# Kernel tuning notes

Hardware: AMD Instinct MI355X
Metric: run time of the kernel (lower is better)

Reference implementation:

```python
import jax, jax.numpy as jnp
import numpy as np

N = 8192
IN = 128   # in_channels
CH = 64    # conv_ch


def setup_inputs() -> dict:
    key = jax.random.key(0)
    ks = jax.random.split(key, 8)
    p = lambda k, shape: jax.random.normal(k, shape, jnp.float32) * 0.02
    return {
        "x": jax.random.normal(ks[0], (N, IN), jnp.float32),
        "edge_index": jax.random.randint(ks[1], (N, N), 0, 2, jnp.int32),
        "W1": p(ks[2], (IN, CH)),      "b1": jnp.zeros((CH,), jnp.float32),
        "W2": p(ks[3], (CH, 2 * CH)),  "b2": jnp.zeros((2 * CH,), jnp.float32),
        "We": p(ks[4], (2 * CH, CH)),  "be": jnp.zeros((CH,), jnp.float32),
        "Wd1": p(ks[5], (2 * CH, CH)), "bd1": jnp.zeros((CH,), jnp.float32),
        "Wd2": p(ks[6], (CH, IN)),     "bd2": jnp.zeros((IN,), jnp.float32),
    }


def _norm_adj(edge_index):
    # PyG GCNConv: A_hat = A + I (self loops appended), sym norm D^-1/2 A_hat D^-1/2
    A = (edge_index != 0).astype(jnp.float32)
    A = A + jnp.eye(A.shape[0], dtype=jnp.float32)
    deg = A.sum(axis=1)
    dinv = jnp.where(deg > 0.0, jax.lax.rsqrt(deg), 0.0)
    return dinv[:, None] * A * dinv[None, :]  # [N, N]


def _gcn(nadj, x, W, b):
    return nadj @ (x @ W) + b


def _lrelu(v):
    return jax.nn.leaky_relu(v, 0.01)  # torch default negative_slope


def reference(x, edge_index, W1, b1, W2, b2, We, be, Wd1, bd1, Wd2, bd2):
    nadj = _norm_adj(edge_index)
    h = _lrelu(_gcn(nadj, x, W1, b1))          # [N, CH]
    z = _lrelu(_gcn(nadj, h, W2, b2))          # [N, 2*CH]
    re = _lrelu(_gcn(nadj, z, We, be))         # [N, CH]
    recon_edge = jax.nn.sigmoid(re @ re.T)     # [N, N]
    xd = _lrelu(_gcn(nadj, z, Wd1, bd1))       # [N, CH]
    x_out = _lrelu(_gcn(nadj, xd, Wd2, bd2))   # [N, IN]
    return (recon_edge, x_out, z)
```

## Files before the change

kernel.cpp:

```cpp
#include <hip/hip_runtime.h>
#include <hip/hip_bf16.h>
#include <stdint.h>

typedef unsigned short u16;
typedef __attribute__((ext_vector_type(8))) short frag8;
typedef __attribute__((ext_vector_type(4))) float f4;

#define N8K 8192
#define SK 8

__device__ __forceinline__ u16 f2bf(float f) {
  union { float f; unsigned u; } v; v.f = f;
  return (u16)((v.u + 0x7FFFu + ((v.u >> 16) & 1u)) >> 16);
}
__device__ __forceinline__ float lrelu(float v) { return v > 0.f ? v : 0.01f * v; }

__device__ __forceinline__ void gld16(const void* g, void* l) {
  __builtin_amdgcn_global_load_lds(
      (__attribute__((address_space(1))) unsigned*)(g),
      (__attribute__((address_space(3))) unsigned*)(l), 16, 0, 0);
}

__global__ __launch_bounds__(256) void k_deg(const int* __restrict__ e,
                                             u16* __restrict__ abf,
                                             float* __restrict__ dinv) {
  int row = blockIdx.x;
  int t = threadIdx.x;
  const int4* er = (const int4*)(e + (size_t)row * N8K);
  ushort4* ar = (ushort4*)(abf + (size_t)row * N8K);
  int cnt = 0;
#pragma unroll
  for (int it = 0; it < 8; ++it) {
    int j4 = it * 256 + t;
    int4 v = er[j4];
    int col = j4 << 2;
    int c0 = (v.x != 0), c1 = (v.y != 0), c2 = (v.z != 0), c3 = (v.w != 0);
    cnt += c0 + c1 + c2 + c3;
    ushort4 a;
    a.x = c0 ? 0x3F80u : 0u;
    a.y = c1 ? 0x3F80u : 0u;
    a.z = c2 ? 0x3F80u : 0u;
    a.w = c3 ? 0x3F80u : 0u;
    if (row >= col && row < col + 4) {
      u16* ap = (u16*)&a;
      int d = row - col;
      ap[d] = ap[d] ? 0x4000u : 0x3F80u;
      cnt += 1;
    }
    ar[j4] = a;
  }
#pragma unroll
  for (int o = 32; o > 0; o >>= 1) cnt += __shfl_down(cnt, o);
  __shared__ int part[4];
  if ((t & 63) == 0) part[t >> 6] = cnt;
  __syncthreads();
  if (t == 0) dinv[row] = 1.0f / sqrtf((float)(part[0] + part[1] + part[2] + part[3]));
}

__global__ __launch_bounds__(256) void k_cvt(const float* __restrict__ x, u16* __restrict__ xb, int n) {
  int i = blockIdx.x * 256 + threadIdx.x;
  if (i < n) xb[i] = f2bf(x[i]);
}

__global__ __launch_bounds__(256) void k_sgemm(const u16* __restrict__ X, int kc, int lkc,
                                               const float* __restrict__ Wa, int wacols,
                                               const float* __restrict__ Wb,
                                               const float* __restrict__ dinv,
                                               u16* __restrict__ Pt) {
  __shared__ __attribute__((aligned(16))) u16 Xs[128 * 128];
  __shared__ __attribute__((aligned(16))) u16 Wt[128 * 128];
  int t = threadIdx.x;
  int mt = blockIdx.x;
  for (int idx = t; idx < (kc << 7); idx += 256) {
    int n = idx >> lkc, k = idx & (kc - 1);
    float v = 0.f;
    if (n < wacols) v = Wa[k * wacols + n];
    else if (Wb)    v = Wb[k * 64 + (n - 64)];
    Wt[(n << lkc) + k] = f2bf(v);
  }
  const u16* gX = X + (size_t)mt * 128 * kc;
  if (kc == 128) {
#pragma unroll
    for (int p = 0; p < 8; ++p) {
      int rr = p * 16 + (t >> 4), sg = t & 15;
      gld16(gX + rr * 128 + sg * 8, Xs + rr * 128 + sg * 8);
    }
  } else {
#pragma unroll
    for (int p = 0; p < 4; ++p) {
      int rr = p * 32 + (t >> 3), sg = t & 7;
      gld16(gX + rr * 64 + sg * 8, Xs + rr * 64 + sg * 8);
    }
  }
  __syncthreads();
  int wave = t >> 6, lane = t & 63;
  int wm = (wave >> 1) * 64, wn = (wave & 1) * 64;
  int fm = lane & 15, fk = (lane >> 4) * 8;
  f4 acc[4][4];
#pragma unroll
  for (int m = 0; m < 4; ++m)
#pragma unroll
    for (int n = 0; n < 4; ++n) acc[m][n] = (f4){0.f, 0.f, 0.f, 0.f};
  for (int ki = 0; ki < kc; ki += 32) {
    frag8 a[4], b[4];
#pragma unroll
    for (int m = 0; m < 4; ++m) a[m] = *(const frag8*)&Xs[(wm + 16 * m + fm) * kc + ki + fk];
#pragma unroll
    for (int n = 0; n < 4; ++n) b[n] = *(const frag8*)&Wt[((wn + 16 * n + fm) << lkc) + ki + fk];
#pragma unroll
    for (int m = 0; m < 4; ++m)
#pragma unroll
      for (int n = 0; n < 4; ++n)
        acc[m][n] = __builtin_amdgcn_mfma_f32_16x16x32_bf16(a[m], b[n], acc[m][n], 0, 0, 0);
  }
  int rbase = (lane >> 4) * 4;
#pragma unroll
  for (int m = 0; m < 4; ++m) {
    int i0 = mt * 128 + wm + 16 * m + rbase;
    float d0 = dinv[i0], d1 = dinv[i0 + 1], d2 = dinv[i0 + 2], d3 = dinv[i0 + 3];
#pragma unroll
    for (int n = 0; n < 4; ++n) {
      int c = wn + 16 * n + fm;
      ushort4 o;
      o.x = f2bf(d0 * acc[m][n][0]);
      o.y = f2bf(d1 * acc[m][n][1]);
      o.z = f2bf(d2 * acc[m][n][2]);
      o.w = f2bf(d3 * acc[m][n][3]);
      *(ushort4*)&Pt[(size_t)c * N8K + i0] = o;
    }
  }
}

__global__ __launch_bounds__(256) void k_bgemm(const u16* __restrict__ A,
                                               const u16* __restrict__ Pt,
                                               float* __restrict__ Ctmp) {
  __shared__ __attribute__((aligned(16))) u16 As[128 * 64];
  __shared__ __attribute__((aligned(16))) u16 Bs[128 * 64];
  int t = threadIdx.x;
  int mt = blockIdx.x, ks = blockIdx.y;
  const int KS = N8K / SK;
  int wave = t >> 6, lane = t & 63;
  int wm = (wave >> 1) * 64, wn = (wave & 1) * 64;
  int fm = lane & 15, fk = (lane >> 4) * 8;
  f4 acc[4][4];
#pragma unroll
  for (int m = 0; m < 4; ++m)
#pragma unroll
    for (int n = 0; n < 4; ++n) acc[m][n] = (f4){0.f, 0.f, 0.f, 0.f};

  int arow = t >> 3, aseg = t & 7;
  const u16* gA0 = A + (size_t)(mt * 128 + arow) * N8K + aseg * 8;
  const u16* gB0 = Pt + (size_t)arow * N8K + aseg * 8;
  u16* lA = As + arow * 64 + aseg * 8;
  u16* lB = Bs + arow * 64 + aseg * 8;

  for (int kk = ks * KS; kk < ks * KS + KS; kk += 64) {
    __syncthreads();
#pragma unroll
    for (int p = 0; p < 4; ++p) {
      gld16(gA0 + (size_t)p * 32 * N8K + kk, lA + p * 32 * 64);
      gld16(gB0 + (size_t)p * 32 * N8K + kk, lB + p * 32 * 64);
    }
    __syncthreads();
#pragma unroll
    for (int ki = 0; ki < 64; ki += 32) {
      frag8 a[4], b[4];
#pragma unroll
      for (int m = 0; m < 4; ++m) a[m] = *(const frag8*)&As[(wm + 16 * m + fm) * 64 + ki + fk];
#pragma unroll
      for (int n = 0; n < 4; ++n) b[n] = *(const frag8*)&Bs[(wn + 16 * n + fm) * 64 + ki + fk];
#pragma unroll
      for (int m = 0; m < 4; ++m)
#pragma unroll
        for (int n = 0; n < 4; ++n)
          acc[m][n] = __builtin_amdgcn_mfma_f32_16x16x32_bf16(a[m], b[n], acc[m][n], 0, 0, 0);
    }
  }
  float* Co = Ctmp + (size_t)ks * N8K * 128;
  int rbase = (lane >> 4) * 4;
#pragma unroll
  for (int m = 0; m < 4; ++m) {
    int i0 = mt * 128 + wm + 16 * m + rbase;
#pragma unroll
    for (int n = 0; n < 4; ++n) {
      int c = wn + 16 * n + fm;
#pragma unroll
      for (int r = 0; r < 4; ++r) Co[(size_t)(i0 + r) * 128 + c] = acc[m][n][r];
    }
  }
}

__global__ __launch_bounds__(256) void k_epi(const float* __restrict__ Ctmp, const float* __restrict__ dinv,
                                             const float* __restrict__ bA, const float* __restrict__ bB,
                                             float* __restrict__ outF, u16* __restrict__ oB1,
                                             u16* __restrict__ oB2, int mode) {
  int idx = blockIdx.x * 256 + threadIdx.x;
  int i = idx >> 7, c = idx & 127;
  float s = 0.f;
#pragma unroll
  for (int k = 0; k < SK; ++k) s += Ctmp[(size_t)k * 1048576 + idx];
  if (mode == 1) {
    if (c < 64) oB1[i * 64 + c] = f2bf(lrelu(dinv[i] * s + bA[c]));
  } else if (mode == 2) {
    float v = lrelu(dinv[i] * s + bA[c]);
    outF[idx] = v;
    oB1[idx] = f2bf(v);
  } else if (mode == 3) {
    if (c < 64) oB1[i * 64 + c] = f2bf(lrelu(dinv[i] * s + bA[c]));
    else        oB2[i * 64 + (c - 64)] = f2bf(lrelu(dinv[i] * s + bB[c - 64]));
  } else {
    outF[idx] = lrelu(dinv[i] * s + bA[c]);
  }
}

__global__ __launch_bounds__(256) void k_recon(const u16* __restrict__ re, float* __restrict__ out) {
  __shared__ __attribute__((aligned(16))) u16 Ra[128 * 64];
  __shared__ __attribute__((aligned(16))) u16 Rb[128 * 64];
  int t = threadIdx.x;
  int bi = blockIdx.x, bj = blockIdx.y;
  int r0 = t >> 3, sg = t & 7;
#pragma unroll
  for (int p = 0; p < 4; ++p) {
    int rr = p * 32 + r0;
    gld16(re + (size_t)(bi * 128 + rr) * 64 + sg * 8, Ra + rr * 64 + sg * 8);
    gld16(re + (size_t)(bj * 128 + rr) * 64 + sg * 8, Rb + rr * 64 + sg * 8);
  }
  __syncthreads();
  int wave = t >> 6, lane = t & 63;
  int wm = (wave >> 1) * 64, wn = (wave & 1) * 64;
  int fm = lane & 15, fk = (lane >> 4) * 8;
  f4 acc[4][4];
#pragma unroll
  for (int m = 0; m < 4; ++m)
#pragma unroll
    for (int n = 0; n < 4; ++n) acc[m][n] = (f4){0.f, 0.f, 0.f, 0.f};
#pragma unroll
  for (int ki = 0; ki < 64; ki += 32) {
    frag8 a[4], b[4];
#pragma unroll
    for (int m = 0; m < 4; ++m) a[m] = *(const frag8*)&Ra[(wm + 16 * m + fm) * 64 + ki + fk];
#pragma unroll
    for (int n = 0; n < 4; ++n) b[n] = *(const frag8*)&Rb[(wn + 16 * n + fm) * 64 + ki + fk];
#pragma unroll
    for (int m = 0; m < 4; ++m)
#pragma unroll
      for (int n = 0; n < 4; ++n)
        acc[m][n] = __builtin_amdgcn_mfma_f32_16x16x32_bf16(a[m], b[n], acc[m][n], 0, 0, 0);
  }
  int rbase = (lane >> 4) * 4;
#pragma unroll
  for (int m = 0; m < 4; ++m) {
#pragma unroll
    for (int n = 0; n < 4; ++n) {
      int gj = bj * 128 + wn + 16 * n + fm;
#pragma unroll
      for (int r = 0; r < 4; ++r) {
        int gi = bi * 128 + wm + 16 * m + rbase + r;
        float v = acc[m][n][r];
        out[(size_t)gi * N8K + gj] = 1.0f / (1.0f + __expf(-v));
      }
    }
  }
}

extern "C" void kernel_launch(void* const* d_in, const int* in_sizes, int n_in,
                              void* d_out, int out_size, void* d_ws, size_t ws_size,
                              hipStream_t stream) {
  const float* x   = (const float*)d_in[0];
  const int*   e   = (const int*)d_in[1];
  const float* W1  = (const float*)d_in[2];
  const float* b1  = (const float*)d_in[3];
  const float* W2  = (const float*)d_in[4];
  const float* b2  = (const float*)d_in[5];
  const float* We  = (const float*)d_in[6];
  const float* be  = (const float*)d_in[7];
  const float* Wd1 = (const float*)d_in[8];
  const float* bd1 = (const float*)d_in[9];
  const float* Wd2 = (const float*)d_in[10];
  const float* bd2 = (const float*)d_in[11];

  float* out       = (float*)d_out;
  float* out_recon = out;
  float* out_x     = out + 67108864;
  float* out_z     = out + 67108864 + 1048576;

  u16*   abf  = (u16*)d_out;
  float* Ctmp = out + 33554432;

  char* ws = (char*)d_ws;
  float* dinv = (float*)(ws);
  u16* Pt   = (u16*)(ws + 32768);
  u16* xbf  = (u16*)(ws + 32768 + 2097152);
  u16* hbf  = (u16*)(ws + 32768 + 2097152 + 2097152);
  u16* zbf  = (u16*)(ws + 32768 + 2097152 + 2097152 + 1048576);
  u16* rebf = (u16*)(ws + 32768 + 2097152 + 2097152 + 1048576 + 2097152);
  u16* xdbf = (u16*)(ws + 32768 + 2097152 + 2097152 + 1048576 + 2097152 + 1048576);

  k_deg<<<8192, 256, 0, stream>>>(e, abf, dinv);
  k_cvt<<<4096, 256, 0, stream>>>(x, xbf, 1048576);

  k_sgemm<<<64, 256, 0, stream>>>(xbf, 128, 7, W1, 64, nullptr, dinv, Pt);
  k_bgemm<<<dim3(64, SK), 256, 0, stream>>>(abf, Pt, Ctmp);
  k_epi<<<4096, 256, 0, stream>>>(Ctmp, dinv, b1, nullptr, nullptr, hbf, nullptr, 1);

  k_sgemm<<<64, 256, 0, stream>>>(hbf, 64, 6, W2, 128, nullptr, dinv, Pt);
  k_bgemm<<<dim3(64, SK), 256, 0, stream>>>(abf, Pt, Ctmp);
  k_epi<<<4096, 256, 0, stream>>>(Ctmp, dinv, b2, nullptr, out_z, zbf, nullptr, 2);

  k_sgemm<<<64, 256, 0, stream>>>(zbf, 128, 7, We, 64, Wd1, dinv, Pt);
  k_bgemm<<<dim3(64, SK), 256, 0, stream>>>(abf, Pt, Ctmp);
  k_epi<<<4096, 256, 0, stream>>>(Ctmp, dinv, be, bd1, nullptr, rebf, xdbf, 3);

  k_sgemm<<<64, 256, 0, stream>>>(xdbf, 64, 6, Wd2, 128, nullptr, dinv, Pt);
  k_bgemm<<<dim3(64, SK), 256, 0, stream>>>(abf, Pt, Ctmp);
  k_epi<<<4096, 256, 0, stream>>>(Ctmp, dinv, bd2, nullptr, out_x, nullptr, nullptr, 4);

  k_recon<<<dim3(64, 64), 256, 0, stream>>>(rebf, out_recon);
}
```

Before: 746.5 us.

## Pad bgemm LDS, register-prefetch next tile, stage recon output through LDS

The split-K bgemm kernel now pads its LDS rows to 72 elements to avoid bank conflicts. It replaces direct global-to-LDS loads with register prefetching of the next K tile, which overlaps global loads with MFMA compute. The recon kernel stages sigmoid results through an LDS buffer in 32-row chunks so each row is written to global memory as coalesced float4 stores instead of scattered scalar stores. The costs are extra LDS, extra VGPRs for the prefetch registers, and additional barriers in the recon epilogue.

```diff
diff --git a/kernel.cpp b/kernel.cpp
--- a/kernel.cpp
+++ b/kernel.cpp
@@ -8,6 +8,7 @@
 
 #define N8K 8192
 #define SK 8
+#define LDA 72
 
 __device__ __forceinline__ u16 f2bf(float f) {
   union { float f; unsigned u; } v; v.f = f;
@@ -134,8 +135,8 @@
 __global__ __launch_bounds__(256) void k_bgemm(const u16* __restrict__ A,
                                                const u16* __restrict__ Pt,
                                                float* __restrict__ Ctmp) {
-  __shared__ __attribute__((aligned(16))) u16 As[128 * 64];
-  __shared__ __attribute__((aligned(16))) u16 Bs[128 * 64];
+  __shared__ __attribute__((aligned(16))) u16 As[128 * LDA];
+  __shared__ __attribute__((aligned(16))) u16 Bs[128 * LDA];
   int t = threadIdx.x;
   int mt = blockIdx.x, ks = blockIdx.y;
   const int KS = N8K / SK;
@@ -151,24 +152,38 @@
   int arow = t >> 3, aseg = t & 7;
   const u16* gA0 = A + (size_t)(mt * 128 + arow) * N8K + aseg * 8;
   const u16* gB0 = Pt + (size_t)arow * N8K + aseg * 8;
-  u16* lA = As + arow * 64 + aseg * 8;
-  u16* lB = Bs + arow * 64 + aseg * 8;
-
-  for (int kk = ks * KS; kk < ks * KS + KS; kk += 64) {
+  u16* lA = As + arow * LDA + aseg * 8;
+  u16* lB = Bs + arow * LDA + aseg * 8;
+
+  int4 ra[4], rb[4];
+  int k0 = ks * KS, k1 = ks * KS + KS;
+#pragma unroll
+  for (int p = 0; p < 4; ++p) {
+    ra[p] = *(const int4*)(gA0 + (size_t)p * 32 * N8K + k0);
+    rb[p] = *(const int4*)(gB0 + (size_t)p * 32 * N8K + k0);
+  }
+  for (int kk = k0; kk < k1; kk += 64) {
     __syncthreads();
 #pragma unroll
     for (int p = 0; p < 4; ++p) {
-      gld16(gA0 + (size_t)p * 32 * N8K + kk, lA + p * 32 * 64);
-      gld16(gB0 + (size_t)p * 32 * N8K + kk, lB + p * 32 * 64);
+      *(int4*)(lA + p * 32 * LDA) = ra[p];
+      *(int4*)(lB + p * 32 * LDA) = rb[p];
     }
     __syncthreads();
+    if (kk + 64 < k1) {
+#pragma unroll
+      for (int p = 0; p < 4; ++p) {
+        ra[p] = *(const int4*)(gA0 + (size_t)p * 32 * N8K + kk + 64);
+        rb[p] = *(const int4*)(gB0 + (size_t)p * 32 * N8K + kk + 64);
+      }
+    }
 #pragma unroll
     for (int ki = 0; ki < 64; ki += 32) {
       frag8 a[4], b[4];
 #pragma unroll
-      for (int m = 0; m < 4; ++m) a[m] = *(const frag8*)&As[(wm + 16 * m + fm) * 64 + ki + fk];
-#pragma unroll
-      for (int n = 0; n < 4; ++n) b[n] = *(const frag8*)&Bs[(wn + 16 * n + fm) * 64 + ki + fk];
+      for (int m = 0; m < 4; ++m) a[m] = *(const frag8*)&As[(wm + 16 * m + fm) * LDA + ki + fk];
+#pragma unroll
+      for (int n = 0; n < 4; ++n) b[n] = *(const frag8*)&Bs[(wn + 16 * n + fm) * LDA + ki + fk];
 #pragma unroll
       for (int m = 0; m < 4; ++m)
 #pragma unroll
@@ -216,6 +231,7 @@
 __global__ __launch_bounds__(256) void k_recon(const u16* __restrict__ re, float* __restrict__ out) {
   __shared__ __attribute__((aligned(16))) u16 Ra[128 * 64];
   __shared__ __attribute__((aligned(16))) u16 Rb[128 * 64];
+  __shared__ __attribute__((aligned(16))) float Ls[32 * 132];
   int t = threadIdx.x;
   int bi = blockIdx.x, bj = blockIdx.y;
   int r0 = t >> 3, sg = t & 7;
@@ -249,16 +265,30 @@
   }
   int rbase = (lane >> 4) * 4;
 #pragma unroll
-  for (int m = 0; m < 4; ++m) {
-#pragma unroll
-    for (int n = 0; n < 4; ++n) {
-      int gj = bj * 128 + wn + 16 * n + fm;
-#pragma unroll
-      for (int r = 0; r < 4; ++r) {
-        int gi = bi * 128 + wm + 16 * m + rbase + r;
-        float v = acc[m][n][r];
-        out[(size_t)gi * N8K + gj] = 1.0f / (1.0f + __expf(-v));
+  for (int chunk = 0; chunk < 4; ++chunk) {
+    __syncthreads();
+    if (wm == (chunk >> 1) * 64) {
+      int mlo = (chunk & 1) * 2;
+#pragma unroll
+      for (int mm = 0; mm < 2; ++mm) {
+        int m = mlo + mm;
+        int lrow = (16 * m + rbase) & 31;
+#pragma unroll
+        for (int n = 0; n < 4; ++n) {
+          int col = wn + 16 * n + fm;
+#pragma unroll
+          for (int r = 0; r < 4; ++r)
+            Ls[(lrow + r) * 132 + col] = 1.0f / (1.0f + __expf(-acc[m][n][r]));
+        }
       }
+    }
+    __syncthreads();
+#pragma unroll
+    for (int it = 0; it < 4; ++it) {
+      int lr = it * 8 + (t >> 5);
+      int col = (t & 31) * 4;
+      float4 v = *(const float4*)&Ls[lr * 132 + col];
+      *(float4*)&out[(size_t)(bi * 128 + chunk * 32 + lr) * N8K + bj * 128 + col] = v;
     }
   }
 }
```

New measurement: 1.024 ms. +37.1%, slower.

## Store adjacency as bytes and expand to bf16 in registers for GCN GEMMs

Applied to the files above, without the earlier changes.

The normalized adjacency is now stored as one byte per entry (0, 1 or 2) instead of bf16, which halves the bytes the four aggregation GEMMs read. Bytes are widened to bf16 fragments in registers with byte-permute instructions. The aggregation and recon GEMMs drop LDS staging and load MFMA fragments straight from global memory. This gives up shared-memory tiling reuse and the barriers, and relies on caches for reuse of Pt and re across waves.

```diff
diff --git a/kernel.cpp b/kernel.cpp
--- a/kernel.cpp
+++ b/kernel.cpp
@@ -3,6 +3,8 @@
 #include <stdint.h>
 
 typedef unsigned short u16;
+typedef unsigned char u8;
+typedef unsigned int u32;
 typedef __attribute__((ext_vector_type(8))) short frag8;
 typedef __attribute__((ext_vector_type(4))) float f4;
 
@@ -21,33 +23,34 @@
       (__attribute__((address_space(3))) unsigned*)(l), 16, 0, 0);
 }
 
+__device__ __forceinline__ void expand4(u32 w, u32& o0, u32& o1) {
+  u32 hi = __builtin_amdgcn_perm(0u, 0x00403F00u, w);
+  u32 lo = __builtin_amdgcn_perm(0u, 0x00008000u, w);
+  o0 = __builtin_amdgcn_perm(hi, lo, 0x05010400u);
+  o1 = __builtin_amdgcn_perm(hi, lo, 0x07030602u);
+}
+
 __global__ __launch_bounds__(256) void k_deg(const int* __restrict__ e,
-                                             u16* __restrict__ abf,
+                                             u8* __restrict__ ab,
                                              float* __restrict__ dinv) {
   int row = blockIdx.x;
   int t = threadIdx.x;
   const int4* er = (const int4*)(e + (size_t)row * N8K);
-  ushort4* ar = (ushort4*)(abf + (size_t)row * N8K);
+  u32* ar = (u32*)(ab + (size_t)row * N8K);
   int cnt = 0;
 #pragma unroll
   for (int it = 0; it < 8; ++it) {
     int j4 = it * 256 + t;
     int4 v = er[j4];
     int col = j4 << 2;
-    int c0 = (v.x != 0), c1 = (v.y != 0), c2 = (v.z != 0), c3 = (v.w != 0);
-    cnt += c0 + c1 + c2 + c3;
-    ushort4 a;
-    a.x = c0 ? 0x3F80u : 0u;
-    a.y = c1 ? 0x3F80u : 0u;
-    a.z = c2 ? 0x3F80u : 0u;
-    a.w = c3 ? 0x3F80u : 0u;
+    u32 c0 = (v.x != 0), c1 = (v.y != 0), c2 = (v.z != 0), c3 = (v.w != 0);
+    cnt += (int)(c0 + c1 + c2 + c3);
+    u32 w = c0 | (c1 << 8) | (c2 << 16) | (c3 << 24);
     if (row >= col && row < col + 4) {
-      u16* ap = (u16*)&a;
-      int d = row - col;
-      ap[d] = ap[d] ? 0x4000u : 0x3F80u;
+      w += 1u << (8 * (row - col));
       cnt += 1;
     }
-    ar[j4] = a;
+    ar[j4] = w;
   }
 #pragma unroll
   for (int o = 32; o > 0; o >>= 1) cnt += __shfl_down(cnt, o);
@@ -131,11 +134,9 @@
   }
 }
 
-__global__ __launch_bounds__(256) void k_bgemm(const u16* __restrict__ A,
+__global__ __launch_bounds__(256) void k_bgemm(const u8* __restrict__ Ab,
                                                const u16* __restrict__ Pt,
                                                float* __restrict__ Ctmp) {
-  __shared__ __attribute__((aligned(16))) u16 As[128 * 64];
-  __shared__ __attribute__((aligned(16))) u16 Bs[128 * 64];
   int t = threadIdx.x;
   int mt = blockIdx.x, ks = blockIdx.y;
   const int KS = N8K / SK;
@@ -148,34 +149,30 @@
 #pragma unroll
     for (int n = 0; n < 4; ++n) acc[m][n] = (f4){0.f, 0.f, 0.f, 0.f};
 
-  int arow = t >> 3, aseg = t & 7;
-  const u16* gA0 = A + (size_t)(mt * 128 + arow) * N8K + aseg * 8;
-  const u16* gB0 = Pt + (size_t)arow * N8K + aseg * 8;
-  u16* lA = As + arow * 64 + aseg * 8;
-  u16* lB = Bs + arow * 64 + aseg * 8;
-
-  for (int kk = ks * KS; kk < ks * KS + KS; kk += 64) {
-    __syncthreads();
-#pragma unroll
-    for (int p = 0; p < 4; ++p) {
-      gld16(gA0 + (size_t)p * 32 * N8K + kk, lA + p * 32 * 64);
-      gld16(gB0 + (size_t)p * 32 * N8K + kk, lB + p * 32 * 64);
-    }
-    __syncthreads();
-#pragma unroll
-    for (int ki = 0; ki < 64; ki += 32) {
-      frag8 a[4], b[4];
-#pragma unroll
-      for (int m = 0; m < 4; ++m) a[m] = *(const frag8*)&As[(wm + 16 * m + fm) * 64 + ki + fk];
-#pragma unroll
-      for (int n = 0; n < 4; ++n) b[n] = *(const frag8*)&Bs[(wn + 16 * n + fm) * 64 + ki + fk];
-#pragma unroll
-      for (int m = 0; m < 4; ++m)
-#pragma unroll
-        for (int n = 0; n < 4; ++n)
-          acc[m][n] = __builtin_amdgcn_mfma_f32_16x16x32_bf16(a[m], b[n], acc[m][n], 0, 0, 0);
-    }
-  }
+  const u8* pa0 = Ab + (size_t)(mt * 128 + wm + fm) * N8K + ks * KS + fk;
+  const u16* pb0 = Pt + (size_t)(wn + fm) * N8K + ks * KS + fk;
+
+#pragma unroll 2
+  for (int kk = 0; kk < KS; kk += 32) {
+    frag8 a[4], b[4];
+#pragma unroll
+    for (int m = 0; m < 4; ++m) {
+      uint2 w = *(const uint2*)(pa0 + (size_t)(16 * m) * N8K + kk);
+      uint4 r;
+      expand4(w.x, r.x, r.y);
+      expand4(w.y, r.z, r.w);
+      a[m] = *(frag8*)&r;
+    }
+#pragma unroll
+    for (int n = 0; n < 4; ++n)
+      b[n] = *(const frag8*)(pb0 + (size_t)(16 * n) * N8K + kk);
+#pragma unroll
+    for (int m = 0; m < 4; ++m)
+#pragma unroll
+      for (int n = 0; n < 4; ++n)
+        acc[m][n] = __builtin_amdgcn_mfma_f32_16x16x32_bf16(a[m], b[n], acc[m][n], 0, 0, 0);
+  }
+
   float* Co = Ctmp + (size_t)ks * N8K * 128;
   int rbase = (lane >> 4) * 4;
 #pragma unroll
@@ -214,21 +211,13 @@
 }
 
 __global__ __launch_bounds__(256) void k_recon(const u16* __restrict__ re, float* __restrict__ out) {
-  __shared__ __attribute__((aligned(16))) u16 Ra[128 * 64];
-  __shared__ __attribute__((aligned(16))) u16 Rb[128 * 64];
   int t = threadIdx.x;
   int bi = blockIdx.x, bj = blockIdx.y;
-  int r0 = t >> 3, sg = t & 7;
-#pragma unroll
-  for (int p = 0; p < 4; ++p) {
-    int rr = p * 32 + r0;
-    gld16(re + (size_t)(bi * 128 + rr) * 64 + sg * 8, Ra + rr * 64 + sg * 8);
-    gld16(re + (size_t)(bj * 128 + rr) * 64 + sg * 8, Rb + rr * 64 + sg * 8);
-  }
-  __syncthreads();
   int wave = t >> 6, lane = t & 63;
   int wm = (wave >> 1) * 64, wn = (wave & 1) * 64;
   int fm = lane & 15, fk = (lane >> 4) * 8;
+  const u16* pa0 = re + (size_t)(bi * 128 + wm + fm) * 64 + fk;
+  const u16* pb0 = re + (size_t)(bj * 128 + wn + fm) * 64 + fk;
   f4 acc[4][4];
 #pragma unroll
   for (int m = 0; m < 4; ++m)
@@ -238,9 +227,9 @@
   for (int ki = 0; ki < 64; ki += 32) {
     frag8 a[4], b[4];
 #pragma unroll
-    for (int m = 0; m < 4; ++m) a[m] = *(const frag8*)&Ra[(wm + 16 * m + fm) * 64 + ki + fk];
-#pragma unroll
-    for (int n = 0; n < 4; ++n) b[n] = *(const frag8*)&Rb[(wn + 16 * n + fm) * 64 + ki + fk];
+    for (int m = 0; m < 4; ++m) a[m] = *(const frag8*)(pa0 + (size_t)(16 * m) * 64 + ki);
+#pragma unroll
+    for (int n = 0; n < 4; ++n) b[n] = *(const frag8*)(pb0 + (size_t)(16 * n) * 64 + ki);
 #pragma unroll
     for (int m = 0; m < 4; ++m)
 #pragma unroll
@@ -284,8 +273,8 @@
   float* out_x     = out + 67108864;
   float* out_z     = out + 67108864 + 1048576;
 
-  u16*   abf  = (u16*)d_out;
-  float* Ctmp = out + 33554432;
+  u8*    abyte = (u8*)d_out;
+  float* Ctmp  = out + 16777216;
 
   char* ws = (char*)d_ws;
   float* dinv = (float*)(ws);
@@ -296,23 +285,23 @@
   u16* rebf = (u16*)(ws + 32768 + 2097152 + 2097152 + 1048576 + 2097152);
   u16* xdbf = (u16*)(ws + 32768 + 2097152 + 2097152 + 1048576 + 2097152 + 1048576);
 
-  k_deg<<<8192, 256, 0, stream>>>(e, abf, dinv);
+  k_deg<<<8192, 256, 0, stream>>>(e, abyte, dinv);
   k_cvt<<<4096, 256, 0, stream>>>(x, xbf, 1048576);
 
   k_sgemm<<<64, 256, 0, stream>>>(xbf, 128, 7, W1, 64, nullptr, dinv, Pt);
-  k_bgemm<<<dim3(64, SK), 256, 0, stream>>>(abf, Pt, Ctmp);
+  k_bgemm<<<dim3(64, SK), 256, 0, stream>>>(abyte, Pt, Ctmp);
   k_epi<<<4096, 256, 0, stream>>>(Ctmp, dinv, b1, nullptr, nullptr, hbf, nullptr, 1);
 
   k_sgemm<<<64, 256, 0, stream>>>(hbf, 64, 6, W2, 128, nullptr, dinv, Pt);
-  k_bgemm<<<dim3(64, SK), 256, 0, stream>>>(abf, Pt, Ctmp);
+  k_bgemm<<<dim3(64, SK), 256, 0, stream>>>(abyte, Pt, Ctmp);
   k_epi<<<4096, 256, 0, stream>>>(Ctmp, dinv, b2, nullptr, out_z, zbf, nullptr, 2);
 
   k_sgemm<<<64, 256, 0, stream>>>(zbf, 128, 7, We, 64, Wd1, dinv, Pt);
-  k_bgemm<<<dim3(64, SK), 256, 0, stream>>>(abf, Pt, Ctmp);
+  k_bgemm<<<dim3(64, SK), 256, 0, stream>>>(abyte, Pt, Ctmp);
   k_epi<<<4096, 256, 0, stream>>>(Ctmp, dinv, be, bd1, nullptr, rebf, xdbf, 3);
 
   k_sgemm<<<64, 256, 0, stream>>>(xdbf, 64, 6, Wd2, 128, nullptr, dinv, Pt);
-  k_bgemm<<<dim3(64, SK), 256, 0, stream>>>(abf, Pt, Ctmp);
+  k_bgemm<<<dim3(64, SK), 256, 0, stream>>>(abyte, Pt, Ctmp);
   k_epi<<<4096, 256, 0, stream>>>(Ctmp, dinv, bd2, nullptr, out_x, nullptr, nullptr, 4);
 
   k_recon<<<dim3(64, 64), 256, 0, stream>>>(rebf, out_recon);
```

New measurement: 850.1 us. +13.9%, slower.
